# Performance work log

Hardware: AMD Instinct MI355X
Metric: run time of the kernel (lower is better)

Reference implementation:

```python
import jax, jax.numpy as jnp
import numpy as np

B, D, H, O, E = 4096, 1024, 4096, 1024, 8
TOP_K = 2


def setup_inputs() -> dict:
    key = jax.random.key(0)
    ks = jax.random.split(key, 7)
    s = 0.02
    return {
        "expert_input": jax.random.normal(ks[0], (B, D), dtype=jnp.float32),
        "Wg": jax.random.normal(ks[1], (D, E), dtype=jnp.float32) * s,
        "bg": jnp.zeros((E,), dtype=jnp.float32),
        "W1": jax.random.normal(ks[2], (E, D, H), dtype=jnp.float32) * s,
        "b1": jnp.zeros((E, H), dtype=jnp.float32),
        "W2": jax.random.normal(ks[3], (E, H, O), dtype=jnp.float32) * s,
        "b2": jnp.zeros((E, O), dtype=jnp.float32),
    }


def reference(expert_input, Wg, bg, W1, b1, W2, b2):
    x = expert_input                                  # [B, D]
    gate_logits = x @ Wg + bg                         # [B, E]
    topk_logits, topk_idx = jax.lax.top_k(gate_logits, TOP_K)
    topk_w = jax.nn.softmax(topk_logits, axis=1)      # softmax over the k selected logits
    rows = jnp.arange(x.shape[0])[:, None]
    dense_w = jnp.zeros_like(gate_logits).at[rows, topk_idx].set(topk_w)  # [B, E]
    # Dense (all-experts) evaluation; zero gate weight == unrouted, so math
    # matches the masked per-expert loop in the torch module exactly.
    h = jax.nn.relu(jnp.einsum('bd,edh->ebh', x, W1) + b1[:, None, :])    # [E, B, H]
    expert_out = jnp.einsum('ebh,eho->ebo', h, W2) + b2[:, None, :]       # [E, B, O]
    routed = jnp.einsum('be,ebo->bo', dense_w, expert_out)                # [B, O]
    return routed
```

## Files before the change

kernel.cpp:

```cpp
#include <hip/hip_runtime.h>
#include <cstdint>

#define DEVI __device__ __forceinline__

typedef __bf16 bf16x8_t __attribute__((ext_vector_type(8)));
typedef float f32x4_t __attribute__((ext_vector_type(4)));

typedef const __attribute__((address_space(1))) unsigned int* gas_t;
typedef __attribute__((address_space(3))) unsigned int* las_t;

DEVI void glds16(const void* g, void* l) {
  __builtin_amdgcn_global_load_lds((gas_t)g, (las_t)l, 16, 0, 0);
}

DEVI uint16_t f2b(float f) {
  uint32_t u = __builtin_bit_cast(uint32_t, f);
  u += 0x7fffu + ((u >> 16) & 1u);
  return (uint16_t)(u >> 16);
}

static constexpr int MAXT = 72;

DEVI void gate_body(int bid, const float* __restrict__ x,
                    const float* __restrict__ Wg, const float* __restrict__ bg,
                    int* __restrict__ gidx, float* __restrict__ gw,
                    uint16_t* __restrict__ xb) {
  const int lane = threadIdx.x & 63;
  const int b = bid * 4 + (threadIdx.x >> 6);
  float acc[8];
#pragma unroll
  for (int e = 0; e < 8; ++e) acc[e] = 0.f;
  const float* xr = x + (size_t)b * 1024;
  uint16_t* xbr = xb + (size_t)b * 1024;
#pragma unroll
  for (int it = 0; it < 4; ++it) {
    const int d0 = it * 256 + lane * 4;
    float4 xv = *(const float4*)(xr + d0);
    uint64_t pk = (uint64_t)f2b(xv.x) | ((uint64_t)f2b(xv.y) << 16) |
                  ((uint64_t)f2b(xv.z) << 32) | ((uint64_t)f2b(xv.w) << 48);
    *(uint64_t*)(xbr + d0) = pk;
    float xs[4] = {xv.x, xv.y, xv.z, xv.w};
#pragma unroll
    for (int q = 0; q < 4; ++q) {
      const float4* wrow = (const float4*)(Wg + (size_t)(d0 + q) * 8);
      float4 wa = wrow[0], wb = wrow[1];
      acc[0] += xs[q] * wa.x; acc[1] += xs[q] * wa.y;
      acc[2] += xs[q] * wa.z; acc[3] += xs[q] * wa.w;
      acc[4] += xs[q] * wb.x; acc[5] += xs[q] * wb.y;
      acc[6] += xs[q] * wb.z; acc[7] += xs[q] * wb.w;
    }
  }
#pragma unroll
  for (int off = 32; off; off >>= 1)
#pragma unroll
    for (int e = 0; e < 8; ++e) acc[e] += __shfl_xor(acc[e], off, 64);
  if (lane == 0) {
    float l[8];
#pragma unroll
    for (int e = 0; e < 8; ++e) l[e] = acc[e] + bg[e];
    int i0 = 0;
#pragma unroll
    for (int e = 1; e < 8; ++e) if (l[e] > l[i0]) i0 = e;
    int i1 = (i0 == 0) ? 1 : 0;
#pragma unroll
    for (int e = 0; e < 8; ++e) if (e != i0 && l[e] > l[i1]) i1 = e;
    float ex = expf(l[i1] - l[i0]);
    float s = 1.f + ex;
    gidx[2 * b] = i0; gidx[2 * b + 1] = i1;
    gw[2 * b] = 1.f / s; gw[2 * b + 1] = ex / s;
  }
}

DEVI void transpose_body(const float* __restrict__ in, uint16_t* __restrict__ outp,
                         int K, int N, int e, int k0, int n0,
                         uint16_t (*t)[72]) {
  const int r = threadIdx.x >> 2;
  const int c0 = (threadIdx.x & 3) * 16;
  const float* src = in + ((size_t)e * K + k0 + r) * N + n0 + c0;
#pragma unroll
  for (int q = 0; q < 4; ++q) {
    float4 v = *(const float4*)(src + q * 4);
    uint64_t pk = (uint64_t)f2b(v.x) | ((uint64_t)f2b(v.y) << 16) |
                  ((uint64_t)f2b(v.z) << 32) | ((uint64_t)f2b(v.w) << 48);
    *(uint64_t*)&t[r][c0 + q * 4] = pk;
  }
  __syncthreads();
  alignas(16) uint16_t buf[16];
#pragma unroll
  for (int j = 0; j < 16; ++j) buf[j] = t[c0 + j][r];
  uint16_t* dst = outp + ((size_t)e * N + n0 + r) * K + k0 + c0;
  *(uint4*)dst = *(const uint4*)&buf[0];
  *(uint4*)(dst + 8) = *(const uint4*)&buf[8];
}

__global__ __launch_bounds__(256) void moe_m1(const float* __restrict__ x,
    const float* __restrict__ Wg, const float* __restrict__ bg,
    int* __restrict__ gidx, float* __restrict__ gw, uint16_t* __restrict__ xb,
    const float* __restrict__ W1, uint16_t* __restrict__ w1t) {
  __shared__ uint16_t t[64][72];
  const int bid = blockIdx.x;
  if (bid < 1024) {
    gate_body(bid, x, Wg, bg, gidx, gw, xb);
  } else {
    int tt = bid - 1024;
    int e = tt >> 10, rem = tt & 1023;
    int kb = rem >> 6, nb2 = rem & 63;
    transpose_body(W1, w1t, 1024, 4096, e, kb * 64, nb2 * 64, t);
  }
}

__global__ __launch_bounds__(256) void moe_scan2(const int* __restrict__ gidx,
    const float* __restrict__ gw, int* __restrict__ meta,
    int* __restrict__ row_index, float* __restrict__ row_w) {
  __shared__ int cnt[8];
  __shared__ int offs[8];
  __shared__ int fill[8];
  if (threadIdx.x < 8) { cnt[threadIdx.x] = 0; fill[threadIdx.x] = 0; }
  __syncthreads();
  int loc[8] = {0, 0, 0, 0, 0, 0, 0, 0};
  for (int i = threadIdx.x; i < 8192; i += 256) {
    int e = gidx[i];
#pragma unroll
    for (int q = 0; q < 8; ++q) loc[q] += (e == q) ? 1 : 0;
  }
#pragma unroll
  for (int q = 0; q < 8; ++q) if (loc[q]) atomicAdd(&cnt[q], loc[q]);
  __syncthreads();
  if (threadIdx.x == 0) {
    int off = 0, tIdx = 0;
    for (int e = 0; e < 8; ++e) {
      int c = cnt[e];
      meta[e] = c;
      meta[8 + e] = off;
      offs[e] = off;
      int nt = (c + 127) >> 7;
      for (int mt = 0; mt < nt; ++mt) {
        meta[32 + tIdx] = e;
        meta[104 + tIdx] = off + mt * 128;
        meta[176 + tIdx] = off + c;
        ++tIdx;
      }
      off += c;
    }
    meta[16] = off;
    meta[25] = tIdx;
  }
  __syncthreads();
  for (int i = threadIdx.x; i < 8192; i += 256) {
    int e = gidx[i];
    int pos = offs[e] + atomicAdd(&fill[e], 1);
    row_index[pos] = i >> 1;
    row_w[pos] = gw[i];
  }
}

template <int KD, int ND, int MODE>
DEVI void gemm_core(int wg, const uint16_t* __restrict__ Am,
                    const uint16_t* __restrict__ Bt, const float* __restrict__ bias,
                    const int* __restrict__ meta, const int* __restrict__ row_index,
                    const float* __restrict__ row_w, uint16_t* __restrict__ hout,
                    float* __restrict__ out, uint16_t (*As)[4096], uint16_t (*Bs)[4096]) {
  constexpr int NB = ND / 128;
  constexpr int NIT = KD / 32;
  const int nb = wg % NB;
  const int ty = wg / NB;
  if (ty >= meta[25]) return;
  const int e = meta[32 + ty];
  const int pos0 = meta[104 + ty];
  const int vend = meta[176 + ty];

  const int tid = threadIdx.x;
  const int lane = tid & 63;
  const int w = tid >> 6;
  const int wr = w >> 1, wc = w & 1;

  size_t aoff[2], boff[2];
#pragma unroll
  for (int j = 0; j < 2; ++j) {
    int c = j * 256 + tid;
    int row = c >> 2;
    int skc = (c & 3) ^ ((row >> 1) & 3);
    int pos = pos0 + row;
    if (pos > 8191) pos = 8191;
    int ar = (MODE == 1) ? row_index[pos] : pos;
    aoff[j] = ((size_t)ar * KD + (size_t)skc * 8) * 2;
    boff[j] = (((size_t)e * ND + (size_t)nb * 128 + row) * KD + (size_t)skc * 8) * 2;
  }
  const char* Ag = (const char*)Am;
  const char* Bg = (const char*)Bt;

  f32x4_t acc[4][4];
  f32x4_t z;
  z[0] = 0.f; z[1] = 0.f; z[2] = 0.f; z[3] = 0.f;
#pragma unroll
  for (int m = 0; m < 4; ++m)
#pragma unroll
    for (int n = 0; n < 4; ++n) acc[m][n] = z;

  auto stage = [&](int buf, int t) {
#pragma unroll
    for (int j = 0; j < 2; ++j) {
      glds16(Ag + aoff[j] + (size_t)t * 64, &As[buf][(j * 256 + w * 64) * 8]);
      glds16(Bg + boff[j] + (size_t)t * 64, &Bs[buf][(j * 256 + w * 64) * 8]);
    }
  };

  stage(0, 0);
  __syncthreads();
  int cur = 0;
  for (int t = 0; t < NIT; ++t) {
    if (t + 1 < NIT) stage(cur ^ 1, t + 1);
    const uint16_t* Ap = As[cur];
    const uint16_t* Bp = Bs[cur];
    bf16x8_t af[4], bfr[4];
#pragma unroll
    for (int m = 0; m < 4; ++m) {
      int row = wr * 64 + m * 16 + (lane & 15);
      int skc = ((lane >> 4) ^ (row >> 1)) & 3;
      af[m] = *(const bf16x8_t*)(Ap + row * 32 + skc * 8);
    }
#pragma unroll
    for (int n = 0; n < 4; ++n) {
      int row = wc * 64 + n * 16 + (lane & 15);
      int skc = ((lane >> 4) ^ (row >> 1)) & 3;
      bfr[n] = *(const bf16x8_t*)(Bp + row * 32 + skc * 8);
    }
#pragma unroll
    for (int m = 0; m < 4; ++m)
#pragma unroll
      for (int n = 0; n < 4; ++n)
        acc[m][n] = __builtin_amdgcn_mfma_f32_16x16x32_bf16(af[m], bfr[n], acc[m][n], 0, 0, 0);
    __syncthreads();
    cur ^= 1;
  }

  const int cb = nb * 128 + wc * 64;
  if constexpr (MODE == 1) {
#pragma unroll
    for (int m = 0; m < 4; ++m) {
      int pr = pos0 + wr * 64 + m * 16 + ((lane >> 4) << 2);
#pragma unroll
      for (int i = 0; i < 4; ++i) {
        int pos = pr + i;
        if (pos < vend) {
#pragma unroll
          for (int n = 0; n < 4; ++n) {
            int col = cb + n * 16 + (lane & 15);
            float v = acc[m][n][i] + bias[e * ND + col];
            v = fmaxf(v, 0.f);
            hout[(size_t)pos * ND + col] = f2b(v);
          }
        }
      }
    }
  } else {
#pragma unroll
    for (int m = 0; m < 4; ++m) {
      int pr = pos0 + wr * 64 + m * 16 + ((lane >> 4) << 2);
#pragma unroll
      for (int i = 0; i < 4; ++i) {
        int pos = pr + i;
        if (pos < vend) {
          int bi = row_index[pos];
          float wgt = row_w[pos];
          float* orow = out + (size_t)bi * ND;
#pragma unroll
          for (int n = 0; n < 4; ++n) {
            int col = cb + n * 16 + (lane & 15);
            float v = (acc[m][n][i] + bias[e * ND + col]) * wgt;
            atomicAdd(orow + col, v);
          }
        }
      }
    }
  }
}

__global__ __launch_bounds__(256, 4) void moe_m2(const uint16_t* __restrict__ xb,
    const uint16_t* __restrict__ w1t, const float* __restrict__ b1,
    const int* __restrict__ meta, const int* __restrict__ rix,
    const float* __restrict__ rw, uint16_t* __restrict__ h,
    const float* __restrict__ W2, uint16_t* __restrict__ w2t) {
  __shared__ uint16_t As[2][4096];
  __shared__ uint16_t Bs[2][4096];
  const int bid = blockIdx.x;
  if (bid < 2304) {
    constexpr int NWG = 2304;
    constexpr int Q8 = NWG >> 3;
    int wg = (bid & 7) * Q8 + (bid >> 3);
    gemm_core<1024, 4096, 1>(wg, xb, w1t, b1, meta, rix, rw, h, nullptr, As, Bs);
  } else {
    int tt = bid - 2304;
    int e = tt >> 10, rem = tt & 1023;
    int kb = rem >> 4, nb2 = rem & 15;
    transpose_body(W2, w2t, 4096, 1024, e, kb * 64, nb2 * 64,
                   (uint16_t(*)[72]) & As[0][0]);
  }
}

__global__ __launch_bounds__(256, 4) void moe_gemm2(const uint16_t* __restrict__ h,
    const uint16_t* __restrict__ w2t, const float* __restrict__ b2,
    const int* __restrict__ meta, const int* __restrict__ rix,
    const float* __restrict__ rw, float* __restrict__ out) {
  __shared__ uint16_t As[2][4096];
  __shared__ uint16_t Bs[2][4096];
  const int nwg = gridDim.x;
  const int orig = blockIdx.x;
  const int q8 = nwg >> 3, r8 = nwg & 7, xcd = orig & 7, loc = orig >> 3;
  int wg = (xcd < r8 ? xcd * (q8 + 1) : r8 * (q8 + 1) + (xcd - r8) * q8) + loc;
  gemm_core<4096, 1024, 2>(wg, h, w2t, b2, meta, rix, rw, nullptr, out, As, Bs);
}

extern "C" void kernel_launch(void* const* d_in, const int* in_sizes, int n_in,
                              void* d_out, int out_size, void* d_ws, size_t ws_size,
                              hipStream_t stream) {
  const float* x  = (const float*)d_in[0];
  const float* Wg = (const float*)d_in[1];
  const float* bg = (const float*)d_in[2];
  const float* W1 = (const float*)d_in[3];
  const float* b1 = (const float*)d_in[4];
  const float* W2 = (const float*)d_in[5];
  const float* b2 = (const float*)d_in[6];
  float* out = (float*)d_out;

  char* ws = (char*)d_ws;
  uint16_t* w1t = (uint16_t*)ws; ws += (size_t)8 * 4096 * 1024 * 2;
  uint16_t* w2t = (uint16_t*)ws; ws += (size_t)8 * 1024 * 4096 * 2;
  uint16_t* xb  = (uint16_t*)ws; ws += (size_t)4096 * 1024 * 2;
  uint16_t* h   = (uint16_t*)ws; ws += (size_t)8192 * 4096 * 2;
  int*   gidx = (int*)ws;   ws += 8192 * 4;
  float* gw   = (float*)ws; ws += 8192 * 4;
  int*   rix  = (int*)ws;   ws += 8192 * 4;
  float* rw   = (float*)ws; ws += 8192 * 4;
  int*   meta = (int*)ws;   ws += 4096;

  hipMemsetAsync(d_out, 0, (size_t)4096 * 1024 * 4, stream);
  moe_m1<<<dim3(1024 + 8192), 256, 0, stream>>>(x, Wg, bg, gidx, gw, xb, W1, w1t);
  moe_scan2<<<dim3(1), 256, 0, stream>>>(gidx, gw, meta, rix, rw);
  moe_m2<<<dim3(2304 + 8192), 256, 0, stream>>>(xb, w1t, b1, meta, rix, rw, h, W2, w2t);
  moe_gemm2<<<dim3(8 * MAXT), 256, 0, stream>>>(h, w2t, b2, meta, rix, rw, out);
}
```

Before: 392.1 us.

## Hand-schedule GEMM main loop with explicit waitcnt, inline LDS reads and setprio

Restructures the double-buffered GEMM K-loop. The next tile is always issued, clamped to the last K-step on the final iteration. Partial vmcnt waits with raw s_barrier replace the full __syncthreads, so the prefetch stays in flight while the current tile is consumed. LDS fragment reads use precomputed swizzled base addresses with ds_read_b128 immediate offsets, and the MFMA block is wrapped in s_setprio. The aim is to cut barrier and address-computation overhead and overlap loads with compute. The cost is fragile inline asm and an assumption about the outstanding-load count.

```diff
diff --git a/kernel.cpp b/kernel.cpp
--- a/kernel.cpp
+++ b/kernel.cpp
@@ -17,6 +17,20 @@
   uint32_t u = __builtin_bit_cast(uint32_t, f);
   u += 0x7fffu + ((u >> 16) & 1u);
   return (uint16_t)(u >> 16);
+}
+
+template <int IMM>
+DEVI f32x4_t ldsr(uint32_t addr) {
+  f32x4_t r;
+  if constexpr (IMM == 0)
+    asm volatile("ds_read_b128 %0, %1" : "=v"(r) : "v"(addr));
+  else if constexpr (IMM == 1024)
+    asm volatile("ds_read_b128 %0, %1 offset:1024" : "=v"(r) : "v"(addr));
+  else if constexpr (IMM == 2048)
+    asm volatile("ds_read_b128 %0, %1 offset:2048" : "=v"(r) : "v"(addr));
+  else
+    asm volatile("ds_read_b128 %0, %1 offset:3072" : "=v"(r) : "v"(addr));
+  return r;
 }
 
 static constexpr int MAXT = 72;
@@ -189,6 +203,14 @@
   const char* Ag = (const char*)Am;
   const char* Bg = (const char*)Bt;
 
+  auto stage = [&](int s, int kt) {
+#pragma unroll
+    for (int j = 0; j < 2; ++j) {
+      glds16(Ag + aoff[j] + (size_t)kt * 64, &As[s][(j * 256 + w * 64) * 8]);
+      glds16(Bg + boff[j] + (size_t)kt * 64, &Bs[s][(j * 256 + w * 64) * 8]);
+    }
+  };
+
   f32x4_t acc[4][4];
   f32x4_t z;
   z[0] = 0.f; z[1] = 0.f; z[2] = 0.f; z[3] = 0.f;
@@ -197,42 +219,41 @@
 #pragma unroll
     for (int n = 0; n < 4; ++n) acc[m][n] = z;
 
-  auto stage = [&](int buf, int t) {
-#pragma unroll
-    for (int j = 0; j < 2; ++j) {
-      glds16(Ag + aoff[j] + (size_t)t * 64, &As[buf][(j * 256 + w * 64) * 8]);
-      glds16(Bg + boff[j] + (size_t)t * 64, &Bs[buf][(j * 256 + w * 64) * 8]);
-    }
-  };
+  const uint32_t skcf = (uint32_t)(((lane >> 4) ^ ((lane & 15) >> 1)) & 3);
+  const uint32_t aB0 = (uint32_t)(size_t)&As[0][0] +
+                       (uint32_t)((wr * 64 + (lane & 15)) * 64) + skcf * 16;
+  const uint32_t bB0 = (uint32_t)(size_t)&Bs[0][0] +
+                       (uint32_t)((wc * 64 + (lane & 15)) * 64) + skcf * 16;
 
   stage(0, 0);
-  __syncthreads();
-  int cur = 0;
   for (int t = 0; t < NIT; ++t) {
-    if (t + 1 < NIT) stage(cur ^ 1, t + 1);
-    const uint16_t* Ap = As[cur];
-    const uint16_t* Bp = Bs[cur];
-    bf16x8_t af[4], bfr[4];
-#pragma unroll
-    for (int m = 0; m < 4; ++m) {
-      int row = wr * 64 + m * 16 + (lane & 15);
-      int skc = ((lane >> 4) ^ (row >> 1)) & 3;
-      af[m] = *(const bf16x8_t*)(Ap + row * 32 + skc * 8);
-    }
-#pragma unroll
-    for (int n = 0; n < 4; ++n) {
-      int row = wc * 64 + n * 16 + (lane & 15);
-      int skc = ((lane >> 4) ^ (row >> 1)) & 3;
-      bfr[n] = *(const bf16x8_t*)(Bp + row * 32 + skc * 8);
-    }
+    int tc = t + 1; if (tc > NIT - 1) tc = NIT - 1;
+    stage((t + 1) & 1, tc);
+    asm volatile("s_waitcnt vmcnt(4)" ::: "memory");
+    __builtin_amdgcn_s_barrier();
+
+    const uint32_t aA = aB0 + (uint32_t)((t & 1) * 8192);
+    const uint32_t bA = bB0 + (uint32_t)((t & 1) * 8192);
+    f32x4_t av[4], bv[4];
+    av[0] = ldsr<0>(aA); av[1] = ldsr<1024>(aA);
+    av[2] = ldsr<2048>(aA); av[3] = ldsr<3072>(aA);
+    bv[0] = ldsr<0>(bA); bv[1] = ldsr<1024>(bA);
+    bv[2] = ldsr<2048>(bA); bv[3] = ldsr<3072>(bA);
+    asm volatile("s_waitcnt lgkmcnt(0)" ::: "memory");
+    __builtin_amdgcn_sched_barrier(0);
+
+    __builtin_amdgcn_s_setprio(1);
 #pragma unroll
     for (int m = 0; m < 4; ++m)
 #pragma unroll
       for (int n = 0; n < 4; ++n)
-        acc[m][n] = __builtin_amdgcn_mfma_f32_16x16x32_bf16(af[m], bfr[n], acc[m][n], 0, 0, 0);
-    __syncthreads();
-    cur ^= 1;
-  }
+        acc[m][n] = __builtin_amdgcn_mfma_f32_16x16x32_bf16(
+            __builtin_bit_cast(bf16x8_t, av[m]), __builtin_bit_cast(bf16x8_t, bv[n]),
+            acc[m][n], 0, 0, 0);
+    __builtin_amdgcn_s_setprio(0);
+    __builtin_amdgcn_s_barrier();
+  }
+  asm volatile("s_waitcnt vmcnt(0)" ::: "memory");
 
   const int cb = nb * 128 + wc * 64;
   if constexpr (MODE == 1) {
```

New measurement: 400.9 us. 1.02x slower.
